# Optimization experiments

Hardware: AMD Instinct MI355X
Metric: run time of the kernel (lower is better)

## Reference

```python
import jax, jax.numpy as jnp
import numpy as np

BIT = 4
VALS_PER_WORD = 32 // BIT  # 8 nibbles per int32 word


def _unpack4(qweight):
    """Unpack 4-bit values: qweight [R, O] int32 -> intweight [R*8, O] int32 in [0,15].
    Row r*8+j comes from nibble j of word r (value j was packed with << 4*j)."""
    shifts = (4 * jnp.arange(VALS_PER_WORD, dtype=jnp.int32))[None, :, None]  # [1,8,1]
    w = (qweight[:, None, :] >> shifts) & 0xF  # [R, 8, O]
    R = qweight.shape[0]
    return w.reshape(R * VALS_PER_WORD, qweight.shape[1])  # [infeatures, outfeatures]


def setup_inputs() -> dict:
    key = jax.random.key(0)
    k1, k2, k3, k4, k5 = jax.random.split(key, 5)
    IN, OUT = 8192, 8192
    x = jax.random.normal(k1, (1, IN), dtype=jnp.float32)
    # random packed words -> uniform random 4-bit nibbles
    qweight = jax.random.randint(k2, (IN * BIT // 32, OUT), 0, 2**31 - 1, dtype=jnp.int32)
    scales = jax.random.uniform(k3, (OUT, 1), dtype=jnp.float32, minval=0.01, maxval=0.05)
    zeros = jax.random.normal(k4, (OUT, 1), dtype=jnp.float32) * 0.02
    bias = jax.random.normal(k5, (OUT,), dtype=jnp.float32)
    return {"x": x, "qweight": qweight, "scales": scales, "zeros": zeros, "bias": bias}


def reference(x, qweight, scales, zeros, bias):
    # Fused dequant + single-token matvec (GPTQ vecquant4matmul semantics):
    # y[o] = bias[o] + sum_k x[k] * (scales[o] * w_int[k, o] - zeros[o])
    w = _unpack4(qweight).astype(jnp.float32)          # [IN, OUT]
    xw = x @ w                                          # [1, OUT]
    xsum = jnp.sum(x, axis=-1, keepdims=True)           # [1, 1]
    y = bias[None, :] + scales[:, 0][None, :] * xw - zeros[:, 0][None, :] * xsum
    return y  # [1, OUT]
```

## Files before the change

kernel.cpp:

```cpp
#include <hip/hip_runtime.h>
#include <stdint.h>

#define THREADS 256
#define COLS_PER_THREAD 4
#define COLS_PER_BLOCK (THREADS * COLS_PER_THREAD)
#define RW 16
#define KSPLIT 64
#define OUTF 8192
#define NPART (KSPLIT * OUTF)

__device__ __forceinline__ float dot8(const float* __restrict__ xr, uint32_t w, float acc) {
    uint32_t lo = w & 0x0F0F0F0Fu;
    uint32_t hi = (w >> 4) & 0x0F0F0F0Fu;
    acc = fmaf(xr[0], (float)(lo & 0xFFu),         acc);
    acc = fmaf(xr[1], (float)(hi & 0xFFu),         acc);
    acc = fmaf(xr[2], (float)((lo >> 8) & 0xFFu),  acc);
    acc = fmaf(xr[3], (float)((hi >> 8) & 0xFFu),  acc);
    acc = fmaf(xr[4], (float)((lo >> 16) & 0xFFu), acc);
    acc = fmaf(xr[5], (float)((hi >> 16) & 0xFFu), acc);
    acc = fmaf(xr[6], (float)(lo >> 24),           acc);
    acc = fmaf(xr[7], (float)(hi >> 24),           acc);
    return acc;
}

__global__ __launch_bounds__(THREADS) void qmatvec4_partial(
    const float* __restrict__ x,
    const uint32_t* __restrict__ qw,
    float* __restrict__ ws)
{
    const int col = blockIdx.x * COLS_PER_BLOCK + threadIdx.x * COLS_PER_THREAD;
    const int kb  = blockIdx.y;
    const int r0  = kb * RW;
    const uint4* qv = (const uint4*)qw;

    float acc0 = 0.f, acc1 = 0.f, acc2 = 0.f, acc3 = 0.f;
    float xs = 0.f;

    #pragma unroll
    for (int i = 0; i < RW; ++i) {
        const int r = r0 + i;
        float xr[8];
        #pragma unroll
        for (int j = 0; j < 8; ++j) {
            xr[j] = x[r * 8 + j];
            xs += xr[j];
        }
        uint4 w = qv[(size_t)r * (OUTF / 4) + (col >> 2)];
        acc0 = dot8(xr, w.x, acc0);
        acc1 = dot8(xr, w.y, acc1);
        acc2 = dot8(xr, w.z, acc2);
        acc3 = dot8(xr, w.w, acc3);
    }

    float4 p = make_float4(acc0, acc1, acc2, acc3);
    ((float4*)ws)[((size_t)kb * OUTF + col) >> 2] = p;

    if (threadIdx.x == 0 && blockIdx.x == 0)
        ws[NPART + kb] = xs;
}

__global__ __launch_bounds__(THREADS) void qmatvec4_reduce(
    const float* __restrict__ ws,
    const float* __restrict__ scales,
    const float* __restrict__ zeros,
    const float* __restrict__ bias,
    float* __restrict__ out)
{
    const int col = blockIdx.x * THREADS + threadIdx.x;

    float xsum = 0.f;
    #pragma unroll
    for (int kb = 0; kb < KSPLIT; ++kb)
        xsum += ws[NPART + kb];

    float s = 0.f;
    #pragma unroll 16
    for (int kb = 0; kb < KSPLIT; ++kb)
        s += ws[(size_t)kb * OUTF + col];

    out[col] = fmaf(scales[col], s, bias[col]) - zeros[col] * xsum;
}

extern "C" void kernel_launch(void* const* d_in, const int* in_sizes, int n_in,
                              void* d_out, int out_size, void* d_ws, size_t ws_size,
                              hipStream_t stream) {
    const float*    x      = (const float*)d_in[0];
    const uint32_t* qw     = (const uint32_t*)d_in[1];
    const float*    scales = (const float*)d_in[2];
    const float*    zeros  = (const float*)d_in[3];
    const float*    bias   = (const float*)d_in[4];
    float*          out    = (float*)d_out;
    float*          ws     = (float*)d_ws;

    dim3 gridA(OUTF / COLS_PER_BLOCK, KSPLIT);
    qmatvec4_partial<<<gridA, THREADS, 0, stream>>>(x, qw, ws);

    qmatvec4_reduce<<<OUTF / THREADS, THREADS, 0, stream>>>(ws, scales, zeros, bias, out);
}
```

Before: 89.40 us.

## Fuse split-K partial and reduce kernels into single block-level reduction kernel

Replaces the two-kernel split-K scheme, which wrote a 64x8192 partial-sum workspace to global memory and reduced it in a second launch, with one kernel. Each 512-thread block owns 32 output columns and stages x in shared memory. Its threads stride over all 1024 packed rows and reduce partials through LDS before applying scale, zero and bias. This removes the workspace round-trip and one launch. In exchange, each wave's weight loads cover only 128-byte row segments, only 256 blocks are launched, and the LDS footprint is large.

```diff
diff --git a/kernel.cpp b/kernel.cpp
--- a/kernel.cpp
+++ b/kernel.cpp
@@ -1,84 +1,96 @@
 #include <hip/hip_runtime.h>
 #include <stdint.h>
 
-#define THREADS 256
-#define COLS_PER_THREAD 4
-#define COLS_PER_BLOCK (THREADS * COLS_PER_THREAD)
-#define RW 16
-#define KSPLIT 64
+
+#define THREADS 512
+#define COLS_PER_BLOCK 32
+#define ROWS 1024
 #define OUTF 8192
-#define NPART (KSPLIT * OUTF)
+#define RG 64
+#define ITERS (ROWS / RG)
 
-__device__ __forceinline__ float dot8(const float* __restrict__ xr, uint32_t w, float acc) {
+__device__ __forceinline__ float dot8(const float4& xa, const float4& xb,
+                                      uint32_t w, float acc) {
     uint32_t lo = w & 0x0F0F0F0Fu;
     uint32_t hi = (w >> 4) & 0x0F0F0F0Fu;
-    acc = fmaf(xr[0], (float)(lo & 0xFFu),         acc);
-    acc = fmaf(xr[1], (float)(hi & 0xFFu),         acc);
-    acc = fmaf(xr[2], (float)((lo >> 8) & 0xFFu),  acc);
-    acc = fmaf(xr[3], (float)((hi >> 8) & 0xFFu),  acc);
-    acc = fmaf(xr[4], (float)((lo >> 16) & 0xFFu), acc);
-    acc = fmaf(xr[5], (float)((hi >> 16) & 0xFFu), acc);
-    acc = fmaf(xr[6], (float)(lo >> 24),           acc);
-    acc = fmaf(xr[7], (float)(hi >> 24),           acc);
+    acc = fmaf(xa.x, (float)(lo & 0xFFu),         acc);
+    acc = fmaf(xa.y, (float)(hi & 0xFFu),         acc);
+    acc = fmaf(xa.z, (float)((lo >> 8) & 0xFFu),  acc);
+    acc = fmaf(xa.w, (float)((hi >> 8) & 0xFFu),  acc);
+    acc = fmaf(xb.x, (float)((lo >> 16) & 0xFFu), acc);
+    acc = fmaf(xb.y, (float)((hi >> 16) & 0xFFu), acc);
+    acc = fmaf(xb.z, (float)(lo >> 24),           acc);
+    acc = fmaf(xb.w, (float)(hi >> 24),           acc);
     return acc;
 }
 
-__global__ __launch_bounds__(THREADS) void qmatvec4_partial(
+__global__ __launch_bounds__(THREADS) void qmatvec4_fused(
     const float* __restrict__ x,
     const uint32_t* __restrict__ qw,
-    float* __restrict__ ws)
-{
-    const int col = blockIdx.x * COLS_PER_BLOCK + threadIdx.x * COLS_PER_THREAD;
-    const int kb  = blockIdx.y;
-    const int r0  = kb * RW;
-    const uint4* qv = (const uint4*)qw;
-
-    float acc0 = 0.f, acc1 = 0.f, acc2 = 0.f, acc3 = 0.f;
-    float xs = 0.f;
-
-    #pragma unroll
-    for (int i = 0; i < RW; ++i) {
-        const int r = r0 + i;
-        float xr[8];
-        #pragma unroll
-        for (int j = 0; j < 8; ++j) {
-            xr[j] = x[r * 8 + j];
-            xs += xr[j];
-        }
-        uint4 w = qv[(size_t)r * (OUTF / 4) + (col >> 2)];
-        acc0 = dot8(xr, w.x, acc0);
-        acc1 = dot8(xr, w.y, acc1);
-        acc2 = dot8(xr, w.z, acc2);
-        acc3 = dot8(xr, w.w, acc3);
-    }
-
-    float4 p = make_float4(acc0, acc1, acc2, acc3);
-    ((float4*)ws)[((size_t)kb * OUTF + col) >> 2] = p;
-
-    if (threadIdx.x == 0 && blockIdx.x == 0)
-        ws[NPART + kb] = xs;
-}
-
-__global__ __launch_bounds__(THREADS) void qmatvec4_reduce(
-    const float* __restrict__ ws,
     const float* __restrict__ scales,
     const float* __restrict__ zeros,
     const float* __restrict__ bias,
     float* __restrict__ out)
 {
-    const int col = blockIdx.x * THREADS + threadIdx.x;
+    __shared__ float4 xs4[ROWS * 2];
+    __shared__ float  red[RG][COLS_PER_BLOCK];
+    __shared__ float  wred[THREADS / 64];
 
-    float xsum = 0.f;
+    const int tid = threadIdx.x;
+    const int ck  = tid & 7;
+    const int rg  = tid >> 3;
+    const int c0  = blockIdx.x * COLS_PER_BLOCK;
+
+    const float4* xg = (const float4*)x;
     #pragma unroll
-    for (int kb = 0; kb < KSPLIT; ++kb)
-        xsum += ws[NPART + kb];
+    for (int i = 0; i < 4; ++i)
+        xs4[tid + i * THREADS] = xg[tid + i * THREADS];
+    __syncthreads();
 
-    float s = 0.f;
-    #pragma unroll 16
-    for (int kb = 0; kb < KSPLIT; ++kb)
-        s += ws[(size_t)kb * OUTF + col];
+    const uint4* qv = (const uint4*)qw;
+    float a0 = 0.f, a1 = 0.f, a2 = 0.f, a3 = 0.f;
+    #pragma unroll
+    for (int it = 0; it < ITERS; ++it) {
+        const int r = rg + it * RG;
+        float4 xa = xs4[r * 2];
+        float4 xb = xs4[r * 2 + 1];
+        uint4 w = qv[(size_t)r * (OUTF / 4) + (c0 >> 2) + ck];
+        a0 = dot8(xa, xb, w.x, a0);
+        a1 = dot8(xa, xb, w.y, a1);
+        a2 = dot8(xa, xb, w.z, a2);
+        a3 = dot8(xa, xb, w.w, a3);
+    }
 
-    out[col] = fmaf(scales[col], s, bias[col]) - zeros[col] * xsum;
+    *(float4*)&red[rg][ck * 4] = make_float4(a0, a1, a2, a3);
+
+    float xs = 0.f;
+    #pragma unroll
+    for (int i = 0; i < 4; ++i) {
+        float4 v = xs4[tid + i * THREADS];
+        xs += v.x + v.y + v.z + v.w;
+    }
+    #pragma unroll
+    for (int off = 32; off; off >>= 1)
+        xs += __shfl_down(xs, off);
+    if ((tid & 63) == 0)
+        wred[tid >> 6] = xs;
+
+    __syncthreads();
+
+    if (tid < COLS_PER_BLOCK) {
+        float xsum = 0.f;
+        #pragma unroll
+        for (int wv = 0; wv < THREADS / 64; ++wv)
+            xsum += wred[wv];
+
+        float s = 0.f;
+        #pragma unroll
+        for (int g = 0; g < RG; ++g)
+            s += red[g][tid];
+
+        const int c = c0 + tid;
+        out[c] = fmaf(scales[c], s, bias[c]) - zeros[c] * xsum;
+    }
 }
 
 extern "C" void kernel_launch(void* const* d_in, const int* in_sizes, int n_in,
@@ -90,10 +102,8 @@
     const float*    zeros  = (const float*)d_in[3];
     const float*    bias   = (const float*)d_in[4];
     float*          out    = (float*)d_out;
-    float*          ws     = (float*)d_ws;
+    (void)d_ws; (void)ws_size;
 
-    dim3 gridA(OUTF / COLS_PER_BLOCK, KSPLIT);
-    qmatvec4_partial<<<gridA, THREADS, 0, stream>>>(x, qw, ws);
-
-    qmatvec4_reduce<<<OUTF / THREADS, THREADS, 0, stream>>>(ws, scales, zeros, bias, out);
+    qmatvec4_fused<<<dim3(OUTF / COLS_PER_BLOCK), THREADS, 0, stream>>>(
+        x, qw, scales, zeros, bias, out);
 }
```

Measured after the change: 86.52 us. 3.2% less time.
